# Kernel tuning notes

Hardware: AMD Instinct MI355X
Metric: run time of the kernel (lower is better)

## Reference

```python
import jax, jax.numpy as jnp
import numpy as np

W = 128      # window_size
BACK = 1     # look_backward
FWD = 0      # look_forward (causal)


def _look_around(x, backward=BACK, forward=FWD, pad_value=-1):
    t = x.shape[1]
    pads = [(0, 0), (backward, forward)] + [(0, 0)] * (x.ndim - 2)
    p = jnp.pad(x, pads, constant_values=pad_value)
    return jnp.concatenate([p[:, i:i + t] for i in range(forward + backward + 1)], axis=2)


def setup_inputs() -> dict:
    key = jax.random.key(0)
    kq, kk, kv = jax.random.split(key, 3)
    B, H, T, D = 4, 8, 8192, 64
    q = jax.random.normal(kq, (B, H, T, D), jnp.float32)
    k = jax.random.normal(kk, (B, H, T, D), jnp.float32)
    v = jax.random.normal(kv, (B, H, T, D), jnp.float32)
    return {"q": q, "k": k, "v": v}


def reference(q, k, v):
    B, H, T, D = q.shape
    win = T // W
    # flatten batch/head, split into windows
    bq = q.reshape(B * H, win, W, D)
    bk = k.reshape(B * H, win, W, D)
    bv = v.reshape(B * H, win, W, D)
    bk = _look_around(bk)
    bv = _look_around(bv)

    bq_t = jnp.arange(T, dtype=jnp.int32).reshape(1, win, W)       # query positions
    bq_k = _look_around(bq_t, pad_value=-1)                        # key positions (pad = -1)

    scale = D ** -0.5
    dots = jnp.einsum('bwid,bwjd->bwij', bq, bk) * scale
    mask_value = -jnp.finfo(dots.dtype).max

    causal_mask = bq_t[:, :, :, None] < bq_k[:, :, None, :]
    pad_mask = (bq_k == -1)[:, :, None, :]
    dots = jnp.where(causal_mask | pad_mask, mask_value, dots)

    attn = jax.nn.softmax(dots, axis=-1)
    out = jnp.einsum('bwij,bwjd->bwid', attn, bv)
    return out.reshape(B, H, T, D)
```

## Files before the change

kernel.cpp:

```cpp
#include <hip/hip_runtime.h>
#include <hip/hip_bf16.h>

typedef __bf16 bf16x8 __attribute__((ext_vector_type(8)));
typedef __bf16 bf16x4 __attribute__((ext_vector_type(4)));
typedef float  f32x4  __attribute__((ext_vector_type(4)));

#define TQ   8192
#define DD   64
#define WW   128
#define PSTR 264

__global__ __launch_bounds__(512, 2)
void lattn_kernel(const float* __restrict__ q, const float* __restrict__ k,
                  const float* __restrict__ v, float* __restrict__ out)
{
    __shared__ __bf16 Klds[256 * 64];
    __shared__ __bf16 Vt[64 * PSTR];
    __shared__ __bf16 Plds[8 * 16 * PSTR];

    const int bx   = blockIdx.x;
    const int bh   = bx >> 6;
    const int w    = bx & 63;
    const int tid  = threadIdx.x;
    const int lane = tid & 63;
    const int wv   = tid >> 6;
    const int q15  = lane & 15;
    const int g    = lane >> 4;

    const size_t base = ((size_t)bh * TQ + (size_t)w * WW) * DD;
    const int    krow0 = w * WW - WW;
    const bool   w0    = (w == 0);

    const int qrow = wv * 16 + q15;
    const float* qp = q + base + (size_t)qrow * DD + g * 8;
    f32x4 q0a = *(const f32x4*)(qp);
    f32x4 q0b = *(const f32x4*)(qp + 4);
    f32x4 q1a = *(const f32x4*)(qp + 32);
    f32x4 q1b = *(const f32x4*)(qp + 36);
    bf16x8 qa0, qa1;
    #pragma unroll
    for (int e = 0; e < 4; ++e) {
        qa0[e]     = (__bf16)q0a[e];
        qa0[4 + e] = (__bf16)q0b[e];
        qa1[e]     = (__bf16)q1a[e];
        qa1[4 + e] = (__bf16)q1b[e];
    }

    #pragma unroll
    for (int it = 0; it < 8; ++it) {
        int flat4 = it * 512 + tid;
        int j  = flat4 >> 4;
        int d0 = (flat4 & 15) * 4;
        int gk = krow0 + j;
        f32x4 val = (f32x4){0.f, 0.f, 0.f, 0.f};
        if (gk >= 0) val = *(const f32x4*)(k + ((size_t)bh * TQ + gk) * DD + d0);
        bf16x4 b;
        #pragma unroll
        for (int e = 0; e < 4; ++e) b[e] = (__bf16)val[e];
        *(bf16x4*)&Klds[j * 64 + (d0 ^ ((j & 7) << 3))] = b;
    }

    #pragma unroll
    for (int it = 0; it < 8; ++it) {
        int R  = it * 8 + wv;
        int jb = R >> 2, db = R & 3;
        int j  = jb * 16 + q15;
        int d0 = db * 16 + g * 4;
        int gv = krow0 + j;
        f32x4 val = (f32x4){0.f, 0.f, 0.f, 0.f};
        if (gv >= 0) val = *(const f32x4*)(v + ((size_t)bh * TQ + gv) * DD + d0);
        #pragma unroll
        for (int c = 0; c < 4; ++c) Vt[(d0 + c) * PSTR + j] = (__bf16)val[c];
    }
    __syncthreads();

    f32x4 accS[16];
    #pragma unroll
    for (int t = 0; t < 16; ++t) accS[t] = (f32x4){0.f, 0.f, 0.f, 0.f};
    #pragma unroll
    for (int t = 0; t < 16; ++t) {
        int j  = t * 16 + q15;
        int rb = j * 64;
        int sw = (j & 7) << 3;
        bf16x8 kb0 = *(const bf16x8*)&Klds[rb + ((g * 8) ^ sw)];
        bf16x8 kb1 = *(const bf16x8*)&Klds[rb + ((32 + g * 8) ^ sw)];
        accS[t] = __builtin_amdgcn_mfma_f32_16x16x32_bf16(qa0, kb0, accS[t], 0, 0, 0);
        accS[t] = __builtin_amdgcn_mfma_f32_16x16x32_bf16(qa1, kb1, accS[t], 0, 0, 0);
    }

    const float SCALE = 0.125f;
    float mx[4] = {-3.4e38f, -3.4e38f, -3.4e38f, -3.4e38f};
    #pragma unroll
    for (int t = 0; t < 16; ++t) {
        int j = t * 16 + q15;
        #pragma unroll
        for (int r = 0; r < 4; ++r) {
            int i = wv * 16 + g * 4 + r;
            float sv = accS[t][r] * SCALE;
            if ((j > i + 128) || (w0 && j < 128)) sv = -3.0e38f;
            accS[t][r] = sv;
            mx[r] = fmaxf(mx[r], sv);
        }
    }
    #pragma unroll
    for (int mb = 1; mb < 16; mb <<= 1) {
        #pragma unroll
        for (int r = 0; r < 4; ++r) mx[r] = fmaxf(mx[r], __shfl_xor(mx[r], mb, 64));
    }
    float sm[4] = {0.f, 0.f, 0.f, 0.f};
    #pragma unroll
    for (int t = 0; t < 16; ++t) {
        #pragma unroll
        for (int r = 0; r < 4; ++r) {
            float p = __expf(accS[t][r] - mx[r]);
            accS[t][r] = p;
            sm[r] += p;
        }
    }
    #pragma unroll
    for (int mb = 1; mb < 16; mb <<= 1) {
        #pragma unroll
        for (int r = 0; r < 4; ++r) sm[r] += __shfl_xor(sm[r], mb, 64);
    }
    float rs[4];
    #pragma unroll
    for (int r = 0; r < 4; ++r) rs[r] = 1.0f / sm[r];

    __bf16* Pw = &Plds[wv * 16 * PSTR];
    #pragma unroll
    for (int r = 0; r < 4; ++r) {
        int lr = g * 4 + r;
        #pragma unroll
        for (int t = 0; t < 16; ++t) {
            Pw[lr * PSTR + t * 16 + q15] = (__bf16)accS[t][r];
        }
    }
    __syncthreads();

    f32x4 accO[4];
    #pragma unroll
    for (int dt = 0; dt < 4; ++dt) accO[dt] = (f32x4){0.f, 0.f, 0.f, 0.f};
    const __bf16* Pr = &Plds[(wv * 16 + q15) * PSTR];
    #pragma unroll
    for (int s = 0; s < 8; ++s) {
        bf16x8 pa = *(const bf16x8*)&Pr[s * 32 + g * 8];
        #pragma unroll
        for (int dt = 0; dt < 4; ++dt) {
            bf16x8 vb = *(const bf16x8*)&Vt[(dt * 16 + q15) * PSTR + s * 32 + g * 8];
            accO[dt] = __builtin_amdgcn_mfma_f32_16x16x32_bf16(pa, vb, accO[dt], 0, 0, 0);
        }
    }

    float* op = out + base;
    #pragma unroll
    for (int dt = 0; dt < 4; ++dt) {
        #pragma unroll
        for (int r = 0; r < 4; ++r) {
            int i = wv * 16 + g * 4 + r;
            op[(size_t)i * DD + dt * 16 + q15] = accO[dt][r] * rs[r];
        }
    }
}

extern "C" void kernel_launch(void* const* d_in, const int* in_sizes, int n_in,
                              void* d_out, int out_size, void* d_ws, size_t ws_size,
                              hipStream_t stream) {
    const float* q = (const float*)d_in[0];
    const float* k = (const float*)d_in[1];
    const float* v = (const float*)d_in[2];
    float* out = (float*)d_out;
    dim3 grid(32 * 64);
    dim3 block(512);
    lattn_kernel<<<grid, block, 0, stream>>>(q, k, v, out);
}
```

Before: 98.20 us.

## Rewrite local attention as flash-style online softmax with 32x32 MFMA and causal block skipping

Replaces the full 128x256 score tile per block with a loop over 32-key blocks. It uses an online softmax in registers with exp2 and a folded scale, and skips key blocks that are fully masked by causality or lie before window 0. K fragments are loaded straight from global memory into registers instead of staging through LDS, and the P tile is passed between lanes with shuffles instead of through LDS. Blocks shrink to 256 threads with 32 queries per wave, and output goes through an LDS transpose so the global stores are coalesced. The point is to cut LDS use and wasted masked work and to raise occupancy, at the cost of repeated K global loads across waves and a serial loop per wave with an uneven trip count.

```diff
diff --git a/kernel.cpp b/kernel.cpp
--- a/kernel.cpp
+++ b/kernel.cpp
@@ -2,21 +2,27 @@
 #include <hip/hip_bf16.h>
 
 typedef __bf16 bf16x8 __attribute__((ext_vector_type(8)));
-typedef __bf16 bf16x4 __attribute__((ext_vector_type(4)));
 typedef float  f32x4  __attribute__((ext_vector_type(4)));
+typedef float  f32x16 __attribute__((ext_vector_type(16)));
+typedef unsigned int u32x4 __attribute__((ext_vector_type(4)));
 
-#define TQ   8192
-#define DD   64
-#define WW   128
-#define PSTR 264
+#define TQ 8192
+#define DD 64
+#define PSTRV 264
 
-__global__ __launch_bounds__(512, 2)
+static __device__ __forceinline__ unsigned pack2_bf16(float lo, float hi) {
+    unsigned short a = __builtin_bit_cast(unsigned short, (__bf16)lo);
+    unsigned short b = __builtin_bit_cast(unsigned short, (__bf16)hi);
+    return ((unsigned)b << 16) | (unsigned)a;
+}
+
+__global__ __launch_bounds__(256, 4)
 void lattn_kernel(const float* __restrict__ q, const float* __restrict__ k,
                   const float* __restrict__ v, float* __restrict__ out)
 {
-    __shared__ __bf16 Klds[256 * 64];
-    __shared__ __bf16 Vt[64 * PSTR];
-    __shared__ __bf16 Plds[8 * 16 * PSTR];
+    __shared__ __align__(16) unsigned char smem[DD * PSTRV * 2];
+    __bf16* Vt = (__bf16*)smem;
+    float*  Ot = (float*)smem;
 
     const int bx   = blockIdx.x;
     const int bh   = bx >> 6;
@@ -24,140 +30,126 @@
     const int tid  = threadIdx.x;
     const int lane = tid & 63;
     const int wv   = tid >> 6;
-    const int q15  = lane & 15;
-    const int g    = lane >> 4;
+    const int l31  = lane & 31;
+    const int hi   = lane >> 5;
 
-    const size_t base = ((size_t)bh * TQ + (size_t)w * WW) * DD;
-    const int    krow0 = w * WW - WW;
-    const bool   w0    = (w == 0);
+    const size_t base  = ((size_t)bh * TQ + w * 128) * DD;
+    const int    krow0 = w * 128 - 128;
 
-    const int qrow = wv * 16 + q15;
-    const float* qp = q + base + (size_t)qrow * DD + g * 8;
-    f32x4 q0a = *(const f32x4*)(qp);
-    f32x4 q0b = *(const f32x4*)(qp + 4);
-    f32x4 q1a = *(const f32x4*)(qp + 32);
-    f32x4 q1b = *(const f32x4*)(qp + 36);
-    bf16x8 qa0, qa1;
-    #pragma unroll
-    for (int e = 0; e < 4; ++e) {
-        qa0[e]     = (__bf16)q0a[e];
-        qa0[4 + e] = (__bf16)q0b[e];
-        qa1[e]     = (__bf16)q1a[e];
-        qa1[4 + e] = (__bf16)q1b[e];
+    bf16x8 qf[4];
+    {
+        const float* qp = q + base + (size_t)(wv * 32 + l31) * DD + hi * 8;
+        #pragma unroll
+        for (int s = 0; s < 4; ++s) {
+            f32x4 a = *(const f32x4*)(qp + 16 * s);
+            f32x4 b = *(const f32x4*)(qp + 16 * s + 4);
+            #pragma unroll
+            for (int e = 0; e < 4; ++e) { qf[s][e] = (__bf16)a[e]; qf[s][4 + e] = (__bf16)b[e]; }
+        }
     }
 
     #pragma unroll
-    for (int it = 0; it < 8; ++it) {
-        int flat4 = it * 512 + tid;
-        int j  = flat4 >> 4;
-        int d0 = (flat4 & 15) * 4;
-        int gk = krow0 + j;
-        f32x4 val = (f32x4){0.f, 0.f, 0.f, 0.f};
-        if (gk >= 0) val = *(const f32x4*)(k + ((size_t)bh * TQ + gk) * DD + d0);
-        bf16x4 b;
+    for (int it = 0; it < 16; ++it) {
+        int flat = it * 256 + tid;
+        int j  = flat >> 4;
+        int d0 = (flat & 15) * 4;
+        int gr = krow0 + j;
+        f32x4 val = {0.f, 0.f, 0.f, 0.f};
+        if (gr >= 0) val = *(const f32x4*)(v + ((size_t)bh * TQ + gr) * DD + d0);
         #pragma unroll
-        for (int e = 0; e < 4; ++e) b[e] = (__bf16)val[e];
-        *(bf16x4*)&Klds[j * 64 + (d0 ^ ((j & 7) << 3))] = b;
-    }
-
-    #pragma unroll
-    for (int it = 0; it < 8; ++it) {
-        int R  = it * 8 + wv;
-        int jb = R >> 2, db = R & 3;
-        int j  = jb * 16 + q15;
-        int d0 = db * 16 + g * 4;
-        int gv = krow0 + j;
-        f32x4 val = (f32x4){0.f, 0.f, 0.f, 0.f};
-        if (gv >= 0) val = *(const f32x4*)(v + ((size_t)bh * TQ + gv) * DD + d0);
-        #pragma unroll
-        for (int c = 0; c < 4; ++c) Vt[(d0 + c) * PSTR + j] = (__bf16)val[c];
+        for (int c = 0; c < 4; ++c) Vt[(d0 + c) * PSTRV + j] = (__bf16)val[c];
     }
     __syncthreads();
 
-    f32x4 accS[16];
-    #pragma unroll
-    for (int t = 0; t < 16; ++t) accS[t] = (f32x4){0.f, 0.f, 0.f, 0.f};
-    #pragma unroll
-    for (int t = 0; t < 16; ++t) {
-        int j  = t * 16 + q15;
-        int rb = j * 64;
-        int sw = (j & 7) << 3;
-        bf16x8 kb0 = *(const bf16x8*)&Klds[rb + ((g * 8) ^ sw)];
-        bf16x8 kb1 = *(const bf16x8*)&Klds[rb + ((32 + g * 8) ^ sw)];
-        accS[t] = __builtin_amdgcn_mfma_f32_16x16x32_bf16(qa0, kb0, accS[t], 0, 0, 0);
-        accS[t] = __builtin_amdgcn_mfma_f32_16x16x32_bf16(qa1, kb1, accS[t], 0, 0, 0);
+    f32x16 o0 = {}, o1 = {};
+    float m2 = -3.0e38f, lsum = 0.f;
+    const float C = 0.18033688011112042f;
+
+    const int kb0   = (w == 0) ? 4 : 0;
+    const int kbend = wv + 4;
+    for (int kb = kb0; kb <= kbend; ++kb) {
+        f32x16 sacc = {};
+        {
+            const float* kp = k + ((size_t)bh * TQ + (krow0 + kb * 32 + l31)) * DD + hi * 8;
+            #pragma unroll
+            for (int s = 0; s < 4; ++s) {
+                f32x4 a = *(const f32x4*)(kp + 16 * s);
+                f32x4 b = *(const f32x4*)(kp + 16 * s + 4);
+                bf16x8 kf;
+                #pragma unroll
+                for (int e = 0; e < 4; ++e) { kf[e] = (__bf16)a[e]; kf[4 + e] = (__bf16)b[e]; }
+                sacc = __builtin_amdgcn_mfma_f32_32x32x16_bf16(kf, qf[s], sacc, 0, 0, 0);
+            }
+        }
+        float p[16];
+        float locmax = -3.0e38f;
+        const bool partial = (kb == kbend);
+        #pragma unroll
+        for (int r = 0; r < 16; ++r) {
+            float sv = sacc[r] * C;
+            int j = (r & 3) + 8 * (r >> 2) + 4 * hi;
+            if (partial && (j > l31)) sv = -3.0e38f;
+            p[r] = sv;
+            locmax = fmaxf(locmax, sv);
+        }
+        locmax = fmaxf(locmax, __shfl_xor(locmax, 32, 64));
+        float mnew = fmaxf(m2, locmax);
+        float fac  = exp2f(m2 - mnew);
+        float ts = 0.f;
+        #pragma unroll
+        for (int r = 0; r < 16; ++r) { float e = exp2f(p[r] - mnew); p[r] = e; ts += e; }
+        ts += __shfl_xor(ts, 32, 64);
+        lsum = lsum * fac + ts;
+        m2 = mnew;
+        #pragma unroll
+        for (int r = 0; r < 16; ++r) { o0[r] *= fac; o1[r] *= fac; }
+
+        unsigned pk[8], xw[8];
+        #pragma unroll
+        for (int m = 0; m < 8; ++m) pk[m] = pack2_bf16(p[2 * m], p[2 * m + 1]);
+        #pragma unroll
+        for (int m = 0; m < 8; ++m) xw[m] = (unsigned)__shfl_xor((int)pk[m], 32, 64);
+        u32x4 f0, f1;
+        f0[0] = hi ? xw[2] : pk[0]; f0[1] = hi ? xw[3] : pk[1];
+        f0[2] = hi ? pk[2] : xw[0]; f0[3] = hi ? pk[3] : xw[1];
+        f1[0] = hi ? xw[6] : pk[4]; f1[1] = hi ? xw[7] : pk[5];
+        f1[2] = hi ? pk[6] : xw[4]; f1[3] = hi ? pk[7] : xw[5];
+        bf16x8 pf0 = __builtin_bit_cast(bf16x8, f0);
+        bf16x8 pf1 = __builtin_bit_cast(bf16x8, f1);
+
+        const __bf16* vb = &Vt[l31 * PSTRV + kb * 32 + hi * 8];
+        bf16x8 v00 = *(const bf16x8*)(vb);
+        bf16x8 v01 = *(const bf16x8*)(vb + 16);
+        bf16x8 v10 = *(const bf16x8*)(vb + 32 * PSTRV);
+        bf16x8 v11 = *(const bf16x8*)(vb + 32 * PSTRV + 16);
+        o0 = __builtin_amdgcn_mfma_f32_32x32x16_bf16(v00, pf0, o0, 0, 0, 0);
+        o0 = __builtin_amdgcn_mfma_f32_32x32x16_bf16(v01, pf1, o0, 0, 0, 0);
+        o1 = __builtin_amdgcn_mfma_f32_32x32x16_bf16(v10, pf0, o1, 0, 0, 0);
+        o1 = __builtin_amdgcn_mfma_f32_32x32x16_bf16(v11, pf1, o1, 0, 0, 0);
     }
 
-    const float SCALE = 0.125f;
-    float mx[4] = {-3.4e38f, -3.4e38f, -3.4e38f, -3.4e38f};
-    #pragma unroll
-    for (int t = 0; t < 16; ++t) {
-        int j = t * 16 + q15;
+    float rl = 1.0f / lsum;
+    __syncthreads();
+    {
+        int iq = wv * 32 + l31;
         #pragma unroll
-        for (int r = 0; r < 4; ++r) {
-            int i = wv * 16 + g * 4 + r;
-            float sv = accS[t][r] * SCALE;
-            if ((j > i + 128) || (w0 && j < 128)) sv = -3.0e38f;
-            accS[t][r] = sv;
-            mx[r] = fmaxf(mx[r], sv);
-        }
-    }
-    #pragma unroll
-    for (int mb = 1; mb < 16; mb <<= 1) {
-        #pragma unroll
-        for (int r = 0; r < 4; ++r) mx[r] = fmaxf(mx[r], __shfl_xor(mx[r], mb, 64));
-    }
-    float sm[4] = {0.f, 0.f, 0.f, 0.f};
-    #pragma unroll
-    for (int t = 0; t < 16; ++t) {
-        #pragma unroll
-        for (int r = 0; r < 4; ++r) {
-            float p = __expf(accS[t][r] - mx[r]);
-            accS[t][r] = p;
-            sm[r] += p;
-        }
-    }
-    #pragma unroll
-    for (int mb = 1; mb < 16; mb <<= 1) {
-        #pragma unroll
-        for (int r = 0; r < 4; ++r) sm[r] += __shfl_xor(sm[r], mb, 64);
-    }
-    float rs[4];
-    #pragma unroll
-    for (int r = 0; r < 4; ++r) rs[r] = 1.0f / sm[r];
-
-    __bf16* Pw = &Plds[wv * 16 * PSTR];
-    #pragma unroll
-    for (int r = 0; r < 4; ++r) {
-        int lr = g * 4 + r;
-        #pragma unroll
-        for (int t = 0; t < 16; ++t) {
-            Pw[lr * PSTR + t * 16 + q15] = (__bf16)accS[t][r];
+        for (int r = 0; r < 16; ++r) {
+            int d = (r & 3) + 8 * (r >> 2) + 4 * hi;
+            Ot[d * 132 + iq]        = o0[r] * rl;
+            Ot[(d + 32) * 132 + iq] = o1[r] * rl;
         }
     }
     __syncthreads();
-
-    f32x4 accO[4];
-    #pragma unroll
-    for (int dt = 0; dt < 4; ++dt) accO[dt] = (f32x4){0.f, 0.f, 0.f, 0.f};
-    const __bf16* Pr = &Plds[(wv * 16 + q15) * PSTR];
-    #pragma unroll
-    for (int s = 0; s < 8; ++s) {
-        bf16x8 pa = *(const bf16x8*)&Pr[s * 32 + g * 8];
+    {
+        int iq = tid >> 1;
+        int dh = (tid & 1) * 32;
+        float* op = out + base + (size_t)iq * DD + dh;
         #pragma unroll
-        for (int dt = 0; dt < 4; ++dt) {
-            bf16x8 vb = *(const bf16x8*)&Vt[(dt * 16 + q15) * PSTR + s * 32 + g * 8];
-            accO[dt] = __builtin_amdgcn_mfma_f32_16x16x32_bf16(pa, vb, accO[dt], 0, 0, 0);
-        }
-    }
-
-    float* op = out + base;
-    #pragma unroll
-    for (int dt = 0; dt < 4; ++dt) {
-        #pragma unroll
-        for (int r = 0; r < 4; ++r) {
-            int i = wv * 16 + g * 4 + r;
-            op[(size_t)i * DD + dt * 16 + q15] = accO[dt][r] * rs[r];
+        for (int u = 0; u < 8; ++u) {
+            f32x4 val;
+            #pragma unroll
+            for (int c = 0; c < 4; ++c) val[c] = Ot[(dh + u * 4 + c) * 132 + iq];
+            *(f32x4*)(op + u * 4) = val;
         }
     }
 }
@@ -170,6 +162,6 @@
     const float* v = (const float*)d_in[2];
     float* out = (float*)d_out;
     dim3 grid(32 * 64);
-    dim3 block(512);
+    dim3 block(256);
     lattn_kernel<<<grid, block, 0, stream>>>(q, k, v, out);
 }
```

New measurement: 90.01 us. 1.09x faster.
